# Performance work log

Hardware: AMD Instinct MI355X
Metric: run time of the kernel (lower is better)

The kernel has to match this reference:

```python
import jax, jax.numpy as jnp
import numpy as np

N, E = 20000, 320000
IN_DIM = 18            # 2 (pos) + k_feat=16
P = 32                 # in_proj_out
H1, D1 = 8, 32         # gat1 heads, head_dim (out_dim = P*heads = 256)
OUT = P * H1           # 256
BD, H2, D2 = 256, 8, 32  # bottleneck dim / heads / head_dim
NID = 1000             # num_real_ids
NEG_SLOPE = 0.2


def _ln(x, g, b, eps=1e-5):
    mu = x.mean(-1, keepdims=True)
    v = ((x - mu) ** 2).mean(-1, keepdims=True)
    return (x - mu) * jax.lax.rsqrt(v + eps) * g + b


def _segment_softmax(score, dst, n):
    # score: [E, H], softmax over edges sharing the same dst node
    m = jax.ops.segment_max(score, dst, num_segments=n)
    e = jnp.exp(score - m[dst])
    s = jax.ops.segment_sum(e, dst, num_segments=n)
    return e / (s[dst] + 1e-16)


def _gatv2(x, src, dst, ea, Wl, Wr, We, att, bias, n, h, d):
    # GATv2 (PyG semantics): e_ij = att . leaky_relu(Wl x_j + Wr x_i + We e_ij)
    xl = (x @ Wl).reshape(n, h, d)           # source transform
    xr = (x @ Wr).reshape(n, h, d)           # target transform
    xe = (ea @ We).reshape(-1, h, d)         # edge embedding [E,h,d]
    f = jax.nn.leaky_relu(xl[src] + xr[dst] + xe, NEG_SLOPE)  # [E,h,d]
    score = jnp.einsum('ehd,hd->eh', f, att)                   # [E,h]
    alpha = _segment_softmax(score, dst, n)                    # [E,h]
    out = jax.ops.segment_sum(alpha[:, :, None] * xl[src], dst, num_segments=n)
    return out.reshape(n, h * d) + bias


def setup_inputs() -> dict:
    key = jax.random.key(0)
    ks = jax.random.split(key, 20)
    s = 0.05
    rn = lambda k, shape: (jax.random.normal(k, shape, jnp.float32) * s)
    return {
        'x_gnn': jax.random.normal(ks[0], (N, IN_DIM), jnp.float32),
        'edge_index': jax.random.randint(ks[1], (2, E), 0, N),
        'edge_attr': jax.random.uniform(ks[2], (E, 1), dtype=jnp.float32),
        'W_in': rn(ks[3], (IN_DIM, P)), 'b_in': jnp.zeros((P,), jnp.float32),
        'Wl1': rn(ks[4], (P, OUT)), 'Wr1': rn(ks[5], (P, OUT)),
        'We1': rn(ks[6], (1, OUT)), 'att1': rn(ks[7], (H1, D1)),
        'bg1': jnp.zeros((OUT,), jnp.float32),
        'ln1_g': jnp.ones((OUT,), jnp.float32), 'ln1_b': jnp.zeros((OUT,), jnp.float32),
        'W_down': rn(ks[8], (OUT, BD)),
        'lnd_g': jnp.ones((BD,), jnp.float32), 'lnd_b': jnp.zeros((BD,), jnp.float32),
        'Wl2': rn(ks[9], (BD, BD)), 'Wr2': rn(ks[10], (BD, BD)),
        'We2': rn(ks[11], (1, BD)), 'att2': rn(ks[12], (H2, D2)),
        'bg2': jnp.zeros((BD,), jnp.float32),
        'ln2_g': jnp.ones((BD,), jnp.float32), 'ln2_b': jnp.zeros((BD,), jnp.float32),
        'W_up': rn(ks[13], (BD, OUT)),
        'lnu_g': jnp.ones((OUT,), jnp.float32), 'lnu_b': jnp.zeros((OUT,), jnp.float32),
        'W_cls': rn(ks[14], (OUT, NID)), 'b_cls': jnp.zeros((NID,), jnp.float32),
    }


def reference(x_gnn, edge_index, edge_attr, W_in, b_in,
              Wl1, Wr1, We1, att1, bg1, ln1_g, ln1_b,
              W_down, lnd_g, lnd_b,
              Wl2, Wr2, We2, att2, bg2, ln2_g, ln2_b,
              W_up, lnu_g, lnu_b, W_cls, b_cls):
    src, dst = edge_index[0], edge_index[1]
    h0 = x_gnn @ W_in + b_in
    # GATv2Block 1: conv + LN (no residual, 32 -> 256)
    g1 = _gatv2(h0, src, dst, edge_attr, Wl1, Wr1, We1, att1, bg1, N, H1, D1)
    h1 = _ln(g1, ln1_g, ln1_b)
    # bottleneck branch
    z = _ln(h1 @ W_down, lnd_g, lnd_b)
    # GATv2Block 2: conv + residual + LN (256 -> 256)
    g2 = _gatv2(z, src, dst, edge_attr, Wl2, Wr2, We2, att2, bg2, N, H2, D2)
    z2 = _ln(g2 + z, ln2_g, ln2_b)
    h2 = z2 @ W_up                       # up projection (dropout is identity in eval)
    h = _ln(h1 + h2, lnu_g, lnu_b)
    logits = h @ W_cls + b_cls
    return (logits, h)
```

## Files before the change

### kernel.cpp

```cpp
#include <hip/hip_runtime.h>
#include <math.h>

#define N_NODES 20000
#define N_EDGES 320000

typedef __attribute__((ext_vector_type(8))) __bf16 bf16x8;
typedef __attribute__((ext_vector_type(8))) unsigned short ushort8;
typedef __attribute__((ext_vector_type(4))) float floatx4;

__device__ __forceinline__ unsigned short f2b(float f) {
    unsigned int u = __float_as_uint(f);
    unsigned int r = (u + 0x7fffu + ((u >> 16) & 1u)) >> 16;
    return (unsigned short)r;
}
__device__ __forceinline__ float b2f(unsigned short u) {
    return __uint_as_float(((unsigned int)u) << 16);
}

__global__ void k_inproj(const float* __restrict__ x, const float* __restrict__ W,
                         const float* __restrict__ b, unsigned short* __restrict__ h0) {
    int t = blockIdx.x * blockDim.x + threadIdx.x;
    if (t >= N_NODES * 32) return;
    int n = t >> 5, p = t & 31;
    float acc = b[p];
    const float* xr = x + n * 18;
#pragma unroll
    for (int k = 0; k < 18; k++) acc = fmaf(xr[k], W[k * 32 + p], acc);
    h0[t] = f2b(acc);
}

__global__ void k_wcvt_all(const float* __restrict__ Wl1, const float* __restrict__ Wr1,
                           const float* __restrict__ Wdn, const float* __restrict__ Wl2,
                           const float* __restrict__ Wr2, const float* __restrict__ Wup,
                           const float* __restrict__ Wcl,
                           unsigned short* __restrict__ o1, unsigned short* __restrict__ o2,
                           unsigned short* __restrict__ o3, unsigned short* __restrict__ o4,
                           unsigned short* __restrict__ o5, unsigned short* __restrict__ o6,
                           unsigned short* __restrict__ o7) {
    int t = blockIdx.x * blockDim.x + threadIdx.x;
    const float* W; unsigned short* O; int Nd, K, idx;
    if (t < 8192)        { W = Wl1; O = o1; Nd = 256;  K = 32;  idx = t; }
    else if (t < 16384)  { W = Wr1; O = o2; Nd = 256;  K = 32;  idx = t - 8192; }
    else if (t < 81920)  { W = Wdn; O = o3; Nd = 256;  K = 256; idx = t - 16384; }
    else if (t < 147456) { W = Wl2; O = o4; Nd = 256;  K = 256; idx = t - 81920; }
    else if (t < 212992) { W = Wr2; O = o5; Nd = 256;  K = 256; idx = t - 147456; }
    else if (t < 278528) { W = Wup; O = o6; Nd = 256;  K = 256; idx = t - 212992; }
    else if (t < 534528) { W = Wcl; O = o7; Nd = 1000; K = 256; idx = t - 278528; }
    else return;
    int n = idx / K, k = idx % K;
    O[idx] = f2b(W[(size_t)k * Nd + n]);
}

__global__ __launch_bounds__(256) void k_gemm_bf16(
    const unsigned short* __restrict__ A, const unsigned short* __restrict__ Bt,
    float* __restrict__ Cf, unsigned short* __restrict__ Cb,
    const float* __restrict__ bias, int M, int N, int K) {
    __shared__ unsigned short As[8 * 64 * 8];
    __shared__ unsigned short Bs[8 * 64 * 8];
    int tid = threadIdx.x;
    int wave = tid >> 6, lane = tid & 63;
    int wr = wave >> 1, wc = wave & 1;
    int row0 = blockIdx.x * 128, col0 = blockIdx.y * 128;
    floatx4 zero4 = {0.f, 0.f, 0.f, 0.f};
    floatx4 acc[4][4];
#pragma unroll
    for (int i = 0; i < 4; i++)
#pragma unroll
        for (int j = 0; j < 4; j++) acc[i][j] = zero4;
    for (int kb = 0; kb < K; kb += 32) {
#pragma unroll
        for (int q = 0; q < 2; q++) {
            int c = tid * 2 + q;
            int row = c >> 2, koff = (c & 3) * 8;
            int lp = (row & 15) + 16 * (koff >> 3);
            int mt = row >> 4;
            ushort8 va = {0, 0, 0, 0, 0, 0, 0, 0};
            if (row0 + row < M)
                va = *(const ushort8*)(A + (size_t)(row0 + row) * K + kb + koff);
            *(ushort8*)(As + (mt * 64 + lp) * 8) = va;
            ushort8 vb = {0, 0, 0, 0, 0, 0, 0, 0};
            if (col0 + row < N)
                vb = *(const ushort8*)(Bt + (size_t)(col0 + row) * K + kb + koff);
            *(ushort8*)(Bs + (mt * 64 + lp) * 8) = vb;
        }
        __syncthreads();
        bf16x8 af[4], bfr[4];
#pragma unroll
        for (int i = 0; i < 4; i++)
            af[i] = *(const bf16x8*)(As + ((wr * 4 + i) * 64 + lane) * 8);
#pragma unroll
        for (int j = 0; j < 4; j++)
            bfr[j] = *(const bf16x8*)(Bs + ((wc * 4 + j) * 64 + lane) * 8);
#pragma unroll
        for (int i = 0; i < 4; i++)
#pragma unroll
            for (int j = 0; j < 4; j++)
                acc[i][j] = __builtin_amdgcn_mfma_f32_16x16x32_bf16(
                    af[i], bfr[j], acc[i][j], 0, 0, 0);
        __syncthreads();
    }
    int quad = lane >> 4, nl = lane & 15;
#pragma unroll
    for (int i = 0; i < 4; i++) {
#pragma unroll
        for (int j = 0; j < 4; j++) {
            int col = col0 + wc * 64 + j * 16 + nl;
            if (col >= N) continue;
            float bv = bias ? bias[col] : 0.f;
#pragma unroll
            for (int r = 0; r < 4; r++) {
                int rr = row0 + wr * 64 + i * 16 + quad * 4 + r;
                if (rr >= M) continue;
                float v = acc[i][j][r] + bv;
                if (Cf) Cf[(size_t)rr * N + col] = v;
                else Cb[(size_t)rr * N + col] = f2b(v);
            }
        }
    }
}

__global__ void k_hist(const int* __restrict__ dst, int* __restrict__ cnt) {
    int e = blockIdx.x * blockDim.x + threadIdx.x;
    if (e >= N_EDGES) return;
    atomicAdd(cnt + dst[e], 1);
}

__global__ __launch_bounds__(1024) void k_scan(const int* __restrict__ cnt,
                                               int* __restrict__ rowptr,
                                               int* __restrict__ wp, int n) {
    __shared__ int tsum[1024];
    int t = threadIdx.x;
    const int chunk = 20;
    int i0 = t * chunk;
    int local[chunk];
    int s = 0;
#pragma unroll
    for (int j = 0; j < chunk; j++) {
        int i = i0 + j;
        int v = (i < n) ? cnt[i] : 0;
        local[j] = s;
        s += v;
    }
    tsum[t] = s;
    __syncthreads();
    for (int off = 1; off < 1024; off <<= 1) {
        int other = (t >= off) ? tsum[t - off] : 0;
        __syncthreads();
        tsum[t] += other;
        __syncthreads();
    }
    int base = (t > 0) ? tsum[t - 1] : 0;
#pragma unroll
    for (int j = 0; j < chunk; j++) {
        int i = i0 + j;
        if (i < n) {
            int ex = base + local[j];
            rowptr[i] = ex;
            wp[i] = ex;
        }
    }
    if (t == 1023) rowptr[n] = tsum[1023];
}

__global__ void k_fill(const int* __restrict__ src, const int* __restrict__ dst,
                       const float* __restrict__ ea, int* __restrict__ wp,
                       int* __restrict__ srcs, float* __restrict__ eas) {
    int e = blockIdx.x * blockDim.x + threadIdx.x;
    if (e >= N_EDGES) return;
    int p = atomicAdd(wp + dst[e], 1);
    srcs[p] = src[e];
    eas[p] = ea[e];
}

__global__ __launch_bounds__(256) void k_gat_ln(
    const int* __restrict__ rowptr, const int* __restrict__ srcs,
    const float* __restrict__ eas, const unsigned short* __restrict__ xlr,
    const float* __restrict__ We, const float* __restrict__ att,
    const float* __restrict__ vbias, const float* __restrict__ res,
    const float* __restrict__ g, const float* __restrict__ b,
    float* __restrict__ outf, unsigned short* __restrict__ outb) {
    int node = blockIdx.x * 4 + (threadIdx.x >> 6);
    if (node >= N_NODES) return;
    int lane = threadIdx.x & 63;
    int beg = rowptr[node], end = rowptr[node + 1];
    float4 wv = ((const float4*)We)[lane];
    float4 av = ((const float4*)att)[lane];
    ushort4 xru = ((const ushort4*)(xlr + (size_t)node * 512 + 256))[lane];
    float4 rv = make_float4(b2f(xru.x), b2f(xru.y), b2f(xru.z), b2f(xru.w));
    float m = -3.0e38f, l = 0.f;
    float4 acc = make_float4(0.f, 0.f, 0.f, 0.f);
    if (beg < end) {
        int last = end - 1;
        int i1 = (beg + 1 < end) ? beg + 1 : last;
        int i2 = (beg + 2 < end) ? beg + 2 : last;
        int i3 = (beg + 3 < end) ? beg + 3 : last;
        int i4 = (beg + 4 < end) ? beg + 4 : last;
        int i5 = (beg + 5 < end) ? beg + 5 : last;
        int i6 = (beg + 6 < end) ? beg + 6 : last;
        int i7 = (beg + 7 < end) ? beg + 7 : last;
        int s0a = srcs[beg], s0b = srcs[i1];
        int s1a = srcs[i2],  s1b = srcs[i3];
        int s2a = srcs[i4],  s2b = srcs[i5];
        int s3a = srcs[i6],  s3b = srcs[i7];
        float a0a = eas[beg], a0b = eas[i1];
        float a1a = eas[i2],  a1b = eas[i3];
        float a2a = eas[i4],  a2b = eas[i5];
        float a3a = eas[i6],  a3b = eas[i7];
        ushort4 x0a = ((const ushort4*)(xlr + (size_t)s0a * 512))[lane];
        ushort4 x0b = ((const ushort4*)(xlr + (size_t)s0b * 512))[lane];
        ushort4 x1a = ((const ushort4*)(xlr + (size_t)s1a * 512))[lane];
        ushort4 x1b = ((const ushort4*)(xlr + (size_t)s1b * 512))[lane];
        ushort4 x2a = ((const ushort4*)(xlr + (size_t)s2a * 512))[lane];
        ushort4 x2b = ((const ushort4*)(xlr + (size_t)s2b * 512))[lane];
        for (int i = beg; i < end; i += 2) {
            int j8 = (i + 8 < end) ? i + 8 : last;
            int j9 = (i + 9 < end) ? i + 9 : last;
            int s4a = srcs[j8], s4b = srcs[j9];
            float a4a = eas[j8], a4b = eas[j9];
            ushort4 x3a = ((const ushort4*)(xlr + (size_t)s3a * 512))[lane];
            ushort4 x3b = ((const ushort4*)(xlr + (size_t)s3b * 512))[lane];
            float4 lva = make_float4(b2f(x0a.x), b2f(x0a.y), b2f(x0a.z), b2f(x0a.w));
            float4 lvb = make_float4(b2f(x0b.x), b2f(x0b.y), b2f(x0b.z), b2f(x0b.w));
            float f, pa = 0.f, pb = 0.f;
            f = lva.x + rv.x + a0a * wv.x; f = fmaxf(f, 0.2f * f); pa = fmaf(f, av.x, pa);
            f = lva.y + rv.y + a0a * wv.y; f = fmaxf(f, 0.2f * f); pa = fmaf(f, av.y, pa);
            f = lva.z + rv.z + a0a * wv.z; f = fmaxf(f, 0.2f * f); pa = fmaf(f, av.z, pa);
            f = lva.w + rv.w + a0a * wv.w; f = fmaxf(f, 0.2f * f); pa = fmaf(f, av.w, pa);
            f = lvb.x + rv.x + a0b * wv.x; f = fmaxf(f, 0.2f * f); pb = fmaf(f, av.x, pb);
            f = lvb.y + rv.y + a0b * wv.y; f = fmaxf(f, 0.2f * f); pb = fmaf(f, av.y, pb);
            f = lvb.z + rv.z + a0b * wv.z; f = fmaxf(f, 0.2f * f); pb = fmaf(f, av.z, pb);
            f = lvb.w + rv.w + a0b * wv.w; f = fmaxf(f, 0.2f * f); pb = fmaf(f, av.w, pb);
            pa += __shfl_xor(pa, 1, 64);
            pa += __shfl_xor(pa, 2, 64);
            pa += __shfl_xor(pa, 4, 64);
            pb += __shfl_xor(pb, 1, 64);
            pb += __shfl_xor(pb, 2, 64);
            pb += __shfl_xor(pb, 4, 64);
            if (i + 1 >= end) pb = -3.0e38f;
            float mnew = fmaxf(fmaxf(m, pa), pb);
            float scale = __expf(m - mnew);
            float wa = __expf(pa - mnew);
            float wb = __expf(pb - mnew);
            acc.x = fmaf(acc.x, scale, fmaf(wa, lva.x, wb * lvb.x));
            acc.y = fmaf(acc.y, scale, fmaf(wa, lva.y, wb * lvb.y));
            acc.z = fmaf(acc.z, scale, fmaf(wa, lva.z, wb * lvb.z));
            acc.w = fmaf(acc.w, scale, fmaf(wa, lva.w, wb * lvb.w));
            l = fmaf(l, scale, wa + wb);
            m = mnew;
            x0a = x1a; x0b = x1b; x1a = x2a; x1b = x2b; x2a = x3a; x2b = x3b;
            a0a = a1a; a0b = a1b; a1a = a2a; a1b = a2b; a2a = a3a; a2b = a3b;
            a3a = a4a; a3b = a4b; s3a = s4a; s3b = s4b;
        }
    }
    float inv = 1.0f / (l + 1e-16f);
    float4 vb4 = ((const float4*)vbias)[lane];
    float4 o = make_float4(fmaf(acc.x, inv, vb4.x), fmaf(acc.y, inv, vb4.y),
                           fmaf(acc.z, inv, vb4.z), fmaf(acc.w, inv, vb4.w));
    if (res) {
        float4 r4 = ((const float4*)(res + (size_t)node * 256))[lane];
        o.x += r4.x; o.y += r4.y; o.z += r4.z; o.w += r4.w;
    }
    float sum = o.x + o.y + o.z + o.w;
#pragma unroll
    for (int off = 32; off > 0; off >>= 1) sum += __shfl_xor(sum, off, 64);
    float mean = sum * (1.0f / 256.0f);
    float dx = o.x - mean, dy = o.y - mean, dz = o.z - mean, dw = o.w - mean;
    float sq = dx * dx + dy * dy + dz * dz + dw * dw;
#pragma unroll
    for (int off = 32; off > 0; off >>= 1) sq += __shfl_xor(sq, off, 64);
    float rstd = 1.0f / sqrtf(sq * (1.0f / 256.0f) + 1e-5f);
    float4 gg = ((const float4*)g)[lane];
    float4 bb = ((const float4*)b)[lane];
    float4 o4 = make_float4(dx * rstd * gg.x + bb.x, dy * rstd * gg.y + bb.y,
                            dz * rstd * gg.z + bb.z, dw * rstd * gg.w + bb.w);
    if (outf) ((float4*)(outf + (size_t)node * 256))[lane] = o4;
    if (outb) {
        ushort4 u;
        u.x = f2b(o4.x); u.y = f2b(o4.y); u.z = f2b(o4.z); u.w = f2b(o4.w);
        ((ushort4*)(outb + (size_t)node * 256))[lane] = u;
    }
}

__global__ void k_ln(const float* __restrict__ in, const float* __restrict__ res,
                     const float* __restrict__ vbias, const float* __restrict__ g,
                     const float* __restrict__ b, float* __restrict__ outf,
                     unsigned short* __restrict__ outb, int rows) {
    int gt = blockIdx.x * blockDim.x + threadIdx.x;
    int wid = gt >> 6, lane = threadIdx.x & 63;
    if (wid >= rows) return;
    float4 v = ((const float4*)(in + (size_t)wid * 256))[lane];
    if (res) {
        float4 r = ((const float4*)(res + (size_t)wid * 256))[lane];
        v.x += r.x; v.y += r.y; v.z += r.z; v.w += r.w;
    }
    if (vbias) {
        float4 r = ((const float4*)vbias)[lane];
        v.x += r.x; v.y += r.y; v.z += r.z; v.w += r.w;
    }
    float sum = v.x + v.y + v.z + v.w;
#pragma unroll
    for (int o = 32; o > 0; o >>= 1) sum += __shfl_xor(sum, o, 64);
    float mean = sum * (1.0f / 256.0f);
    float dx = v.x - mean, dy = v.y - mean, dz = v.z - mean, dw = v.w - mean;
    float sq = dx * dx + dy * dy + dz * dz + dw * dw;
#pragma unroll
    for (int o = 32; o > 0; o >>= 1) sq += __shfl_xor(sq, o, 64);
    float inv = 1.0f / sqrtf(sq * (1.0f / 256.0f) + 1e-5f);
    float4 gg = ((const float4*)g)[lane];
    float4 bb = ((const float4*)b)[lane];
    float4 o4 = make_float4(dx * inv * gg.x + bb.x, dy * inv * gg.y + bb.y,
                            dz * inv * gg.z + bb.z, dw * inv * gg.w + bb.w);
    if (outf) ((float4*)(outf + (size_t)wid * 256))[lane] = o4;
    if (outb) {
        ushort4 u;
        u.x = f2b(o4.x); u.y = f2b(o4.y); u.z = f2b(o4.z); u.w = f2b(o4.w);
        ((ushort4*)(outb + (size_t)wid * 256))[lane] = u;
    }
}

extern "C" void kernel_launch(void* const* d_in, const int* in_sizes, int n_in,
                              void* d_out, int out_size, void* d_ws, size_t ws_size,
                              hipStream_t stream) {
    const float* x_gnn = (const float*)d_in[0];
    const int* ei = (const int*)d_in[1];
    const int* src = ei;
    const int* dst = ei + N_EDGES;
    const float* ea   = (const float*)d_in[2];
    const float* W_in = (const float*)d_in[3];
    const float* b_in = (const float*)d_in[4];
    const float* Wl1  = (const float*)d_in[5];
    const float* Wr1  = (const float*)d_in[6];
    const float* We1  = (const float*)d_in[7];
    const float* att1 = (const float*)d_in[8];
    const float* bg1  = (const float*)d_in[9];
    const float* ln1_g = (const float*)d_in[10];
    const float* ln1_b = (const float*)d_in[11];
    const float* W_down = (const float*)d_in[12];
    const float* lnd_g = (const float*)d_in[13];
    const float* lnd_b = (const float*)d_in[14];
    const float* Wl2  = (const float*)d_in[15];
    const float* Wr2  = (const float*)d_in[16];
    const float* We2  = (const float*)d_in[17];
    const float* att2 = (const float*)d_in[18];
    const float* bg2  = (const float*)d_in[19];
    const float* ln2_g = (const float*)d_in[20];
    const float* ln2_b = (const float*)d_in[21];
    const float* W_up = (const float*)d_in[22];
    const float* lnu_g = (const float*)d_in[23];
    const float* lnu_b = (const float*)d_in[24];
    const float* W_cls = (const float*)d_in[25];
    const float* b_cls = (const float*)d_in[26];

    float* ws = (float*)d_ws;
    float* B_agg = ws;
    float* B_h1  = B_agg + 5120000;
    float* B_z   = B_h1 + 5120000;
    unsigned short* B_xlr = (unsigned short*)(B_z + 5120000);
    unsigned short* B_actb = B_xlr + 10240000;
    unsigned short* B_h0b = B_actb + 5120000;
    unsigned short* Wt_l1 = B_h0b + 640000;
    unsigned short* Wt_r1 = Wt_l1 + 8192;
    unsigned short* Wt_down = Wt_r1 + 8192;
    unsigned short* Wt_l2 = Wt_down + 65536;
    unsigned short* Wt_r2 = Wt_l2 + 65536;
    unsigned short* Wt_up = Wt_r2 + 65536;
    unsigned short* Wt_cls = Wt_up + 65536;
    int* C_cnt = (int*)(Wt_cls + 256000 + (256000 & 1));
    int* C_row = C_cnt + 20000;
    int* C_wp  = C_row + 20001;
    int* C_src = C_wp + 20000;
    float* C_ea = (float*)(C_src + 320000);

    float* out_logits = (float*)d_out;
    float* out_h = out_logits + (size_t)N_NODES * 1000;

    int lnblk = (N_NODES * 64 + 255) / 256;
    int gatblk = (N_NODES + 3) / 4;
    dim3 gg((N_NODES + 127) / 128, 2);
    dim3 gl((N_NODES + 127) / 128, 4);
    dim3 gc((N_NODES + 127) / 128, 8);

    hipMemsetAsync(C_cnt, 0, (size_t)20000 * 4, stream);
    k_hist<<<(N_EDGES + 255) / 256, 256, 0, stream>>>(dst, C_cnt);
    k_scan<<<1, 1024, 0, stream>>>(C_cnt, C_row, C_wp, N_NODES);
    k_fill<<<(N_EDGES + 255) / 256, 256, 0, stream>>>(src, dst, ea, C_wp, C_src, C_ea);

    k_wcvt_all<<<(534528 + 255) / 256, 256, 0, stream>>>(
        Wl1, Wr1, W_down, Wl2, Wr2, W_up, W_cls,
        Wt_l1, Wt_r1, Wt_down, Wt_l2, Wt_r2, Wt_up, Wt_cls);

    k_inproj<<<(N_NODES * 32 + 255) / 256, 256, 0, stream>>>(x_gnn, W_in, b_in, B_h0b);
    k_gemm_bf16<<<gl, 256, 0, stream>>>(B_h0b, Wt_l1, nullptr, B_xlr, nullptr, N_NODES, 512, 32);
    k_gat_ln<<<gatblk, 256, 0, stream>>>(C_row, C_src, C_ea, B_xlr, We1, att1,
                                         bg1, nullptr, ln1_g, ln1_b, B_h1, B_actb);
    k_gemm_bf16<<<gg, 256, 0, stream>>>(B_actb, Wt_down, B_agg, nullptr, nullptr, N_NODES, 256, 256);
    k_ln<<<lnblk, 256, 0, stream>>>(B_agg, nullptr, nullptr, lnd_g, lnd_b, B_z, B_actb, N_NODES);
    k_gemm_bf16<<<gl, 256, 0, stream>>>(B_actb, Wt_l2, nullptr, B_xlr, nullptr, N_NODES, 512, 256);
    k_gat_ln<<<gatblk, 256, 0, stream>>>(C_row, C_src, C_ea, B_xlr, We2, att2,
                                         bg2, B_z, ln2_g, ln2_b, nullptr, B_actb);
    k_gemm_bf16<<<gg, 256, 0, stream>>>(B_actb, Wt_up, B_agg, nullptr, nullptr, N_NODES, 256, 256);
    k_ln<<<lnblk, 256, 0, stream>>>(B_agg, B_h1, nullptr, lnu_g, lnu_b, out_h, B_actb, N_NODES);
    k_gemm_bf16<<<gc, 256, 0, stream>>>(B_actb, Wt_cls, out_logits, nullptr, b_cls, N_NODES, 1000, 256);
}
```

Measured before the change: 454.0 us.

## Fuse LayerNorm into a full-width GEMM with LDS-resident swizzled weights

Adds a k_gemm_ln kernel that keeps a whole 256-column by K=256 weight slice in shared memory and streams A straight from global memory into registers, prefetching one k-step ahead. The down and up projections now compute their LayerNorm (and residual add) in the GEMM epilogue through a cross-wave shared reduction. This removes the two standalone k_ln kernels and their fp32 round trips through global memory. The weight conversion kernel now writes XOR-swizzled, zero-padded transposed weights to avoid LDS bank conflicts. The trade-offs are 128KB of LDS per block, which allows only one block per CU, and fewer blocks for the 256-wide GEMMs, which may leave CUs idle.

```diff
diff --git a/kernel.cpp b/kernel.cpp
--- a/kernel.cpp
+++ b/kernel.cpp
@@ -38,17 +38,19 @@
                            unsigned short* __restrict__ o5, unsigned short* __restrict__ o6,
                            unsigned short* __restrict__ o7) {
     int t = blockIdx.x * blockDim.x + threadIdx.x;
-    const float* W; unsigned short* O; int Nd, K, idx;
-    if (t < 8192)        { W = Wl1; O = o1; Nd = 256;  K = 32;  idx = t; }
-    else if (t < 16384)  { W = Wr1; O = o2; Nd = 256;  K = 32;  idx = t - 8192; }
-    else if (t < 81920)  { W = Wdn; O = o3; Nd = 256;  K = 256; idx = t - 16384; }
-    else if (t < 147456) { W = Wl2; O = o4; Nd = 256;  K = 256; idx = t - 81920; }
-    else if (t < 212992) { W = Wr2; O = o5; Nd = 256;  K = 256; idx = t - 147456; }
-    else if (t < 278528) { W = Wup; O = o6; Nd = 256;  K = 256; idx = t - 212992; }
-    else if (t < 534528) { W = Wcl; O = o7; Nd = 1000; K = 256; idx = t - 278528; }
+    const float* W; unsigned short* O; int Nd, K, idx; bool swz;
+    if (t < 8192)        { W = Wl1; O = o1; Nd = 256;  K = 32;  idx = t;          swz = false; }
+    else if (t < 16384)  { W = Wr1; O = o2; Nd = 256;  K = 32;  idx = t - 8192;   swz = false; }
+    else if (t < 81920)  { W = Wdn; O = o3; Nd = 256;  K = 256; idx = t - 16384;  swz = true; }
+    else if (t < 147456) { W = Wl2; O = o4; Nd = 256;  K = 256; idx = t - 81920;  swz = true; }
+    else if (t < 212992) { W = Wr2; O = o5; Nd = 256;  K = 256; idx = t - 147456; swz = true; }
+    else if (t < 278528) { W = Wup; O = o6; Nd = 256;  K = 256; idx = t - 212992; swz = true; }
+    else if (t < 540672) { W = Wcl; O = o7; Nd = 1000; K = 256; idx = t - 278528; swz = true; }
     else return;
     int n = idx / K, k = idx % K;
-    O[idx] = f2b(W[(size_t)k * Nd + n]);
+    float v = (n < Nd) ? W[(size_t)k * Nd + n] : 0.f;
+    int pos = swz ? (n * K + ((((k >> 3) ^ (n & 7)) << 3) | (k & 7))) : idx;
+    O[pos] = f2b(v);
 }
 
 __global__ __launch_bounds__(256) void k_gemm_bf16(
@@ -114,6 +116,157 @@
                 float v = acc[i][j][r] + bv;
                 if (Cf) Cf[(size_t)rr * N + col] = v;
                 else Cb[(size_t)rr * N + col] = f2b(v);
+            }
+        }
+    }
+}
+
+__global__ __launch_bounds__(256, 1) void k_gemm_ln(
+    const unsigned short* __restrict__ A,
+    const unsigned short* __restrict__ Bsw,
+    int M, int Ncols, int ldC,
+    const float* __restrict__ bias,
+    const float* __restrict__ res,
+    const float* __restrict__ g, const float* __restrict__ b,
+    float* __restrict__ outf, unsigned short* __restrict__ outb) {
+    __shared__ unsigned short Bs[256 * 256];
+    __shared__ float red[2][128][2];
+    int tid = threadIdx.x, lane = tid & 63, wave = tid >> 6;
+    int wr = wave >> 1, wc = wave & 1;
+    int nl = lane & 15, quad = lane >> 4;
+    int row0 = blockIdx.x * 128, col0 = blockIdx.y * 256;
+
+    const unsigned short* aptr =
+        A + (size_t)(row0 + wr * 64 + nl) * 256 + quad * 8;
+    bf16x8 a_cur[4], a_nxt[4];
+#pragma unroll
+    for (int i = 0; i < 4; i++) {
+        a_cur[i] = *(const bf16x8*)(aptr + i * 16 * 256);
+        a_nxt[i] = a_cur[i];
+    }
+
+    {
+        const ushort8* bsrc8 = (const ushort8*)(Bsw + (size_t)col0 * 256);
+        ushort8* bdst8 = (ushort8*)Bs;
+#pragma unroll
+        for (int t = 0; t < 32; t++) bdst8[t * 256 + tid] = bsrc8[t * 256 + tid];
+    }
+    __syncthreads();
+
+    floatx4 zero4 = {0.f, 0.f, 0.f, 0.f};
+    floatx4 acc[4][8];
+#pragma unroll
+    for (int i = 0; i < 4; i++)
+#pragma unroll
+        for (int j = 0; j < 8; j++) acc[i][j] = zero4;
+
+    int lcbase = wc * 128 + nl;
+    int swx = lcbase & 7;
+#pragma unroll
+    for (int kb = 0; kb < 8; kb++) {
+        if (kb < 7) {
+#pragma unroll
+            for (int i = 0; i < 4; i++)
+                a_nxt[i] = *(const bf16x8*)(aptr + i * 16 * 256 + (kb + 1) * 32);
+        }
+        int swz_byte = (((kb * 4 + quad) ^ swx) << 4);
+#pragma unroll
+        for (int j = 0; j < 8; j++) {
+            bf16x8 bf = *(const bf16x8*)((const char*)Bs +
+                                         (size_t)(lcbase + j * 16) * 512 + swz_byte);
+#pragma unroll
+            for (int i = 0; i < 4; i++)
+                acc[i][j] = __builtin_amdgcn_mfma_f32_16x16x32_bf16(
+                    a_cur[i], bf, acc[i][j], 0, 0, 0);
+        }
+#pragma unroll
+        for (int i = 0; i < 4; i++) a_cur[i] = a_nxt[i];
+    }
+
+    if (g == nullptr) {
+#pragma unroll
+        for (int j = 0; j < 8; j++) {
+            int col = col0 + wc * 128 + j * 16 + nl;
+            if (col >= Ncols) continue;
+            float bv = bias ? bias[col] : 0.f;
+#pragma unroll
+            for (int i = 0; i < 4; i++) {
+#pragma unroll
+                for (int r = 0; r < 4; r++) {
+                    int rr = row0 + wr * 64 + i * 16 + quad * 4 + r;
+                    if (rr >= M) continue;
+                    float v = acc[i][j][r] + bv;
+                    if (outf) outf[(size_t)rr * ldC + col] = v;
+                    if (outb) outb[(size_t)rr * ldC + col] = f2b(v);
+                }
+            }
+        }
+        return;
+    }
+
+    if (res) {
+#pragma unroll
+        for (int i = 0; i < 4; i++)
+#pragma unroll
+            for (int j = 0; j < 8; j++) {
+                int col = wc * 128 + j * 16 + nl;
+#pragma unroll
+                for (int r = 0; r < 4; r++) {
+                    int rr = row0 + wr * 64 + i * 16 + quad * 4 + r;
+                    acc[i][j][r] += res[(size_t)rr * 256 + col];
+                }
+            }
+    }
+#pragma unroll
+    for (int i = 0; i < 4; i++) {
+#pragma unroll
+        for (int r = 0; r < 4; r++) {
+            float s = 0.f, q = 0.f;
+#pragma unroll
+            for (int j = 0; j < 8; j++) {
+                float v = acc[i][j][r];
+                s += v;
+                q = fmaf(v, v, q);
+            }
+            s += __shfl_xor(s, 1, 64); q += __shfl_xor(q, 1, 64);
+            s += __shfl_xor(s, 2, 64); q += __shfl_xor(q, 2, 64);
+            s += __shfl_xor(s, 4, 64); q += __shfl_xor(q, 4, 64);
+            s += __shfl_xor(s, 8, 64); q += __shfl_xor(q, 8, 64);
+            if (nl == 0) {
+                int lr = wr * 64 + i * 16 + quad * 4 + r;
+                red[wc][lr][0] = s;
+                red[wc][lr][1] = q;
+            }
+        }
+    }
+    __syncthreads();
+    float mean_[4][4], rstd_[4][4];
+#pragma unroll
+    for (int i = 0; i < 4; i++) {
+#pragma unroll
+        for (int r = 0; r < 4; r++) {
+            int lr = wr * 64 + i * 16 + quad * 4 + r;
+            float sum = red[0][lr][0] + red[1][lr][0];
+            float sq = red[0][lr][1] + red[1][lr][1];
+            float mean = sum * (1.0f / 256.0f);
+            float var = sq * (1.0f / 256.0f) - mean * mean;
+            mean_[i][r] = mean;
+            rstd_[i][r] = 1.0f / sqrtf(var + 1e-5f);
+        }
+    }
+#pragma unroll
+    for (int j = 0; j < 8; j++) {
+        int col = wc * 128 + j * 16 + nl;
+        float gv = g[col], bvv = b[col];
+#pragma unroll
+        for (int i = 0; i < 4; i++) {
+#pragma unroll
+            for (int r = 0; r < 4; r++) {
+                int rr = row0 + wr * 64 + i * 16 + quad * 4 + r;
+                if (rr >= M) continue;
+                float o = (acc[i][j][r] - mean_[i][r]) * rstd_[i][r] * gv + bvv;
+                if (outf) outf[(size_t)rr * 256 + col] = o;
+                if (outb) outb[(size_t)rr * 256 + col] = f2b(o);
             }
         }
     }
@@ -281,43 +434,6 @@
     }
 }
 
-__global__ void k_ln(const float* __restrict__ in, const float* __restrict__ res,
-                     const float* __restrict__ vbias, const float* __restrict__ g,
-                     const float* __restrict__ b, float* __restrict__ outf,
-                     unsigned short* __restrict__ outb, int rows) {
-    int gt = blockIdx.x * blockDim.x + threadIdx.x;
-    int wid = gt >> 6, lane = threadIdx.x & 63;
-    if (wid >= rows) return;
-    float4 v = ((const float4*)(in + (size_t)wid * 256))[lane];
-    if (res) {
-        float4 r = ((const float4*)(res + (size_t)wid * 256))[lane];
-        v.x += r.x; v.y += r.y; v.z += r.z; v.w += r.w;
-    }
-    if (vbias) {
-        float4 r = ((const float4*)vbias)[lane];
-        v.x += r.x; v.y += r.y; v.z += r.z; v.w += r.w;
-    }
-    float sum = v.x + v.y + v.z + v.w;
-#pragma unroll
-    for (int o = 32; o > 0; o >>= 1) sum += __shfl_xor(sum, o, 64);
-    float mean = sum * (1.0f / 256.0f);
-    float dx = v.x - mean, dy = v.y - mean, dz = v.z - mean, dw = v.w - mean;
-    float sq = dx * dx + dy * dy + dz * dz + dw * dw;
-#pragma unroll
-    for (int o = 32; o > 0; o >>= 1) sq += __shfl_xor(sq, o, 64);
-    float inv = 1.0f / sqrtf(sq * (1.0f / 256.0f) + 1e-5f);
-    float4 gg = ((const float4*)g)[lane];
-    float4 bb = ((const float4*)b)[lane];
-    float4 o4 = make_float4(dx * inv * gg.x + bb.x, dy * inv * gg.y + bb.y,
-                            dz * inv * gg.z + bb.z, dw * inv * gg.w + bb.w);
-    if (outf) ((float4*)(outf + (size_t)wid * 256))[lane] = o4;
-    if (outb) {
-        ushort4 u;
-        u.x = f2b(o4.x); u.y = f2b(o4.y); u.z = f2b(o4.z); u.w = f2b(o4.w);
-        ((ushort4*)(outb + (size_t)wid * 256))[lane] = u;
-    }
-}
-
 extern "C" void kernel_launch(void* const* d_in, const int* in_sizes, int n_in,
                               void* d_out, int out_size, void* d_ws, size_t ws_size,
                               hipStream_t stream) {
@@ -365,7 +481,7 @@
     unsigned short* Wt_r2 = Wt_l2 + 65536;
     unsigned short* Wt_up = Wt_r2 + 65536;
     unsigned short* Wt_cls = Wt_up + 65536;
-    int* C_cnt = (int*)(Wt_cls + 256000 + (256000 & 1));
+    int* C_cnt = (int*)(Wt_cls + 262144);
     int* C_row = C_cnt + 20000;
     int* C_wp  = C_row + 20001;
     int* C_src = C_wp + 20000;
@@ -374,18 +490,16 @@
     float* out_logits = (float*)d_out;
     float* out_h = out_logits + (size_t)N_NODES * 1000;
 
-    int lnblk = (N_NODES * 64 + 255) / 256;
     int gatblk = (N_NODES + 3) / 4;
-    dim3 gg((N_NODES + 127) / 128, 2);
-    dim3 gl((N_NODES + 127) / 128, 4);
-    dim3 gc((N_NODES + 127) / 128, 8);
+    int gemmM = (N_NODES + 127) / 128;
+    dim3 gl(gemmM, 4);
 
     hipMemsetAsync(C_cnt, 0, (size_t)20000 * 4, stream);
     k_hist<<<(N_EDGES + 255) / 256, 256, 0, stream>>>(dst, C_cnt);
     k_scan<<<1, 1024, 0, stream>>>(C_cnt, C_row, C_wp, N_NODES);
     k_fill<<<(N_EDGES + 255) / 256, 256, 0, stream>>>(src, dst, ea, C_wp, C_src, C_ea);
 
-    k_wcvt_all<<<(534528 + 255) / 256, 256, 0, stream>>>(
+    k_wcvt_all<<<(540672 + 255) / 256, 256, 0, stream>>>(
         Wl1, Wr1, W_down, Wl2, Wr2, W_up, W_cls,
         Wt_l1, Wt_r1, Wt_down, Wt_l2, Wt_r2, Wt_up, Wt_cls);
 
@@ -393,12 +507,15 @@
     k_gemm_bf16<<<gl, 256, 0, stream>>>(B_h0b, Wt_l1, nullptr, B_xlr, nullptr, N_NODES, 512, 32);
     k_gat_ln<<<gatblk, 256, 0, stream>>>(C_row, C_src, C_ea, B_xlr, We1, att1,
                                          bg1, nullptr, ln1_g, ln1_b, B_h1, B_actb);
-    k_gemm_bf16<<<gg, 256, 0, stream>>>(B_actb, Wt_down, B_agg, nullptr, nullptr, N_NODES, 256, 256);
-    k_ln<<<lnblk, 256, 0, stream>>>(B_agg, nullptr, nullptr, lnd_g, lnd_b, B_z, B_actb, N_NODES);
-    k_gemm_bf16<<<gl, 256, 0, stream>>>(B_actb, Wt_l2, nullptr, B_xlr, nullptr, N_NODES, 512, 256);
+    k_gemm_ln<<<dim3(gemmM, 1), 256, 0, stream>>>(
+        B_actb, Wt_down, N_NODES, 256, 256, nullptr, nullptr, lnd_g, lnd_b, B_z, B_actb);
+    k_gemm_ln<<<dim3(gemmM, 2), 256, 0, stream>>>(
+        B_actb, Wt_l2, N_NODES, 512, 512, nullptr, nullptr, nullptr, nullptr, nullptr, B_xlr);
     k_gat_ln<<<gatblk, 256, 0, stream>>>(C_row, C_src, C_ea, B_xlr, We2, att2,
                                          bg2, B_z, ln2_g, ln2_b, nullptr, B_actb);
-    k_gemm_bf16<<<gg, 256, 0, stream>>>(B_actb, Wt_up, B_agg, nullptr, nullptr, N_NODES, 256, 256);
-    k_ln<<<lnblk, 256, 0, stream>>>(B_agg, B_h1, nullptr, lnu_g, lnu_b, out_h, B_actb, N_NODES);
-    k_gemm_bf16<<<gc, 256, 0, stream>>>(B_actb, Wt_cls, out_logits, nullptr, b_cls, N_NODES, 1000, 256);
-}
+    k_gemm_ln<<<dim3(gemmM, 1), 256, 0, stream>>>(
+        B_actb, Wt_up, N_NODES, 256, 256, nullptr, B_h1, lnu_g, lnu_b, out_h, B_actb);
+    k_gemm_ln<<<dim3(gemmM, 4), 256, 0, stream>>>(
+        B_actb, Wt_cls, N_NODES, 1000, 1000, b_cls, nullptr, nullptr, nullptr,
+        out_logits, nullptr);
+}
```

Result: slower. 499.0 us (+9.9%).
